# Performance work log

Hardware: AMD Instinct MI355X
Metric: run time of the kernel (lower is better)

## Reference

```python
import jax, jax.numpy as jnp
import numpy as np

N_NODES = 50000
N_EDGES = 640000
IN_DIM = 128
HID = 128
OUT_DIM = 16
BATCH = 2
EPS = 1e-5


def setup_inputs() -> dict:
    key = jax.random.key(0)
    ks = jax.random.split(key, 12)
    x = jax.random.normal(ks[0], (BATCH, N_NODES, IN_DIM), dtype=jnp.float32)
    edge_index = jax.random.randint(ks[1], (2, N_EDGES), 0, N_NODES, dtype=jnp.int32)
    # learned per-edge log-weights (initialized ~0 like nn.Parameter(zeros), small noise for a nontrivial test)
    edge_weight_param = 0.01 * jax.random.normal(ks[2], (N_EDGES,), dtype=jnp.float32)
    s1 = 1.0 / np.sqrt(IN_DIM)
    s2 = 1.0 / np.sqrt(HID)
    W1 = jax.random.uniform(ks[3], (IN_DIM, HID), minval=-s1, maxval=s1, dtype=jnp.float32)
    b1 = jnp.zeros((HID,), jnp.float32)
    W2 = jax.random.uniform(ks[4], (HID, HID), minval=-s2, maxval=s2, dtype=jnp.float32)
    b2 = jnp.zeros((HID,), jnp.float32)
    g1 = jnp.ones((HID,), jnp.float32); be1 = jnp.zeros((HID,), jnp.float32)
    g2 = jnp.ones((HID,), jnp.float32); be2 = jnp.zeros((HID,), jnp.float32)
    Wc = jax.random.uniform(ks[5], (HID, OUT_DIM), minval=-s2, maxval=s2, dtype=jnp.float32)
    bc = jax.random.uniform(ks[6], (OUT_DIM,), minval=-s2, maxval=s2, dtype=jnp.float32)
    return {"x": x, "edge_index": edge_index, "edge_weight_param": edge_weight_param,
            "W1": W1, "b1": b1, "W2": W2, "b2": b2,
            "g1": g1, "be1": be1, "g2": g2, "be2": be2,
            "Wc": Wc, "bc": bc}


def _gcn_norm(edge_index, edge_weight):
    # PyG GCNConv: add self-loops (weight 1), symmetric D^-1/2 A D^-1/2 normalization
    row = jnp.concatenate([edge_index[0], jnp.arange(N_NODES, dtype=edge_index.dtype)])
    col = jnp.concatenate([edge_index[1], jnp.arange(N_NODES, dtype=edge_index.dtype)])
    ew = jnp.concatenate([edge_weight, jnp.ones((N_NODES,), edge_weight.dtype)])
    deg = jax.ops.segment_sum(ew, col, num_segments=N_NODES)
    dinv = jnp.where(deg > 0, jax.lax.rsqrt(jnp.maximum(deg, 1e-30)), 0.0)
    norm = dinv[row] * ew * dinv[col]
    return row, col, norm


def _gcn_conv(x, W, b, row, col, norm):
    # x: [B, N, F_in] -> [B, N, F_out]; gather-scale-scatter over edges
    xw = x @ W                                   # [B, N, H]
    msg = xw[:, row, :] * norm[None, :, None]    # [B, E+N, H]
    out = jax.vmap(lambda m: jax.ops.segment_sum(m, col, num_segments=N_NODES))(msg)
    return out + b


def _batchnorm(h, gamma, beta):
    # training-mode BN over flattened (B*N) rows, biased variance, eps=1e-5
    B, N, F = h.shape
    hf = h.reshape(-1, F)
    mu = hf.mean(axis=0)
    var = hf.var(axis=0)
    return (((hf - mu) * jax.lax.rsqrt(var + EPS)) * gamma + beta).reshape(B, N, F)


def reference(x, edge_index, edge_weight_param, W1, b1, W2, b2, g1, be1, g2, be2, Wc, bc):
    edge_weight = jnp.exp(edge_weight_param)  # learned exp edge weights
    row, col, norm = _gcn_norm(edge_index, edge_weight)
    h = jax.nn.relu(_gcn_conv(x, W1, b1, row, col, norm))
    h = _batchnorm(h, g1, be1)
    # dropout is identity in eval / deterministic reference
    h = jax.nn.relu(_gcn_conv(h, W2, b2, row, col, norm))
    h = _batchnorm(h, g2, be2)
    return h @ Wc + bc  # [B, N, OUT_DIM]
```

## Files before the change

### kernel.cpp

```cpp
#include <hip/hip_runtime.h>
#include <hip/hip_bf16.h>
#include <cstdint>
#include <cstddef>

#define N_NODES 50000
#define N_EDGES 640000
#define ROWS    100000
#define HID     128
#define OUTD    16
#define AGG_BLOCKS 2048
#define MID_BLOCKS 32
#define SCAN_BLOCKS 196
#define GEMM_BLOCKS 512
#define GEMM_TILES  (ROWS / 16)

typedef __attribute__((ext_vector_type(8))) uint16_t ushort8;
typedef __attribute__((ext_vector_type(8))) __bf16   bf16x8;
typedef __attribute__((ext_vector_type(4))) float    floatx4;

union FragU { ushort8 u; bf16x8 b; };

__device__ __forceinline__ float bf_lo(uint32_t u){
  union { uint32_t u; float f; } c; c.u = u << 16; return c.f;
}
__device__ __forceinline__ float bf_hi(uint32_t u){
  union { uint32_t u; float f; } c; c.u = u & 0xffff0000u; return c.f;
}
__device__ __forceinline__ uint16_t f2bf(float f){
  union { float f; uint32_t u; } c; c.f = f;
  uint32_t u = c.u;
  uint32_t r = (u + 0x7fffu + ((u >> 16) & 1u)) >> 16;
  return (uint16_t)r;
}

__global__ void k_init(unsigned long long* __restrict__ dc){
  int i = blockIdx.x * 256 + threadIdx.x;
  if (i < N_NODES) dc[i] = 0ull;
}

__global__ void k_edge1(const int* __restrict__ ei, const float* __restrict__ ewp,
                        unsigned long long* __restrict__ dc){
  int e = blockIdx.x * 256 + threadIdx.x;
  if (e < N_EDGES){
    float w = expf(ewp[e]);
    int c = ei[N_EDGES + e];
    unsigned long long inc = (1ull << 44) | (unsigned long long)(w * 1048576.0f + 0.5f);
    atomicAdd(&dc[c], inc);
  }
}

__global__ void k_scan_bsum(const unsigned long long* __restrict__ dc, int* __restrict__ bsum,
                            float* __restrict__ dinv){
  __shared__ int sd[256];
  int tid = threadIdx.x;
  int i = blockIdx.x * 256 + tid;
  int cnt = 0;
  if (i < N_NODES){
    unsigned long long v = dc[i];
    cnt = (int)(v >> 44);
    float deg = 1.0f + (float)((double)(v & ((1ull << 44) - 1)) * (1.0 / 1048576.0));
    dinv[i] = 1.0f / sqrtf(deg);
  }
  sd[tid] = cnt;
  __syncthreads();
  for (int off = 128; off > 0; off >>= 1){
    if (tid < off) sd[tid] += sd[tid + off];
    __syncthreads();
  }
  if (tid == 0) bsum[blockIdx.x] = sd[0];
}

__global__ void k_scan_excl(int* __restrict__ bsum){
  __shared__ int sd[256];
  int tid = threadIdx.x;
  sd[tid] = (tid < SCAN_BLOCKS) ? bsum[tid] : 0;
  __syncthreads();
  if (tid == 0){
    int run = 0;
    for (int i = 0; i < SCAN_BLOCKS; i++){ int t = sd[i]; sd[i] = run; run += t; }
  }
  __syncthreads();
  if (tid < SCAN_BLOCKS) bsum[tid] = sd[tid];
}

__global__ void k_scan_write(const unsigned long long* __restrict__ dc, const int* __restrict__ bsum,
                             int* __restrict__ rp, int* __restrict__ cur){
  __shared__ int sd[256];
  int tid = threadIdx.x;
  int i = blockIdx.x * 256 + tid;
  int v = (i < N_NODES) ? (int)(dc[i] >> 44) : 0;
  sd[tid] = v;
  __syncthreads();
  for (int off = 1; off < 256; off <<= 1){
    int t = (tid >= off) ? sd[tid - off] : 0;
    __syncthreads();
    sd[tid] += t;
    __syncthreads();
  }
  if (i < N_NODES){
    int r = bsum[blockIdx.x] + sd[tid] - v;
    rp[i] = r;
    cur[i] = r;
  }
  if (blockIdx.x == 0 && tid == 0) rp[N_NODES] = N_EDGES;
}

__global__ void k_fill(const int* __restrict__ ei, const float* __restrict__ ewp,
                       const float* __restrict__ dinv, int* __restrict__ cur,
                       unsigned long long* __restrict__ edg){
  int e = blockIdx.x * 256 + threadIdx.x;
  if (e < N_EDGES){
    int r = ei[e];
    int c = ei[N_EDGES + e];
    float w = expf(ewp[e]);
    float nrm = dinv[r] * w * dinv[c];
    int p = atomicAdd(&cur[c], 1);
    edg[p] = ((unsigned long long)__float_as_uint(nrm) << 32) | (unsigned int)r;
  }
}

__global__ void k_wpack(const float* __restrict__ W, const float* __restrict__ sca,
                        uint16_t* __restrict__ WP){
  int t = blockIdx.x * 256 + threadIdx.x;
  int L = t & 63;
  int s = (t >> 6) & 3;
  int c = t >> 8;
  int n = c * 16 + (L & 15);
  int k0 = s * 32 + (L >> 4) * 8;
  ushort8 r;
#pragma unroll
  for (int j = 0; j < 8; j++){
    float w = W[(size_t)(k0 + j) * HID + n];
    if (sca) w *= sca[k0 + j];
    r[j] = f2bf(w);
  }
  *((ushort8*)(WP + (size_t)t * 8)) = r;
}

__global__ void k_wpackc(const float* __restrict__ Wc, const float* __restrict__ sca,
                         uint16_t* __restrict__ WPC){
  int t = threadIdx.x;
  int L = t & 63;
  int s = t >> 6;
  int n = L & 15;
  int k0 = s * 32 + (L >> 4) * 8;
  ushort8 r;
#pragma unroll
  for (int j = 0; j < 8; j++)
    r[j] = f2bf(sca[k0 + j] * Wc[(size_t)(k0 + j) * OUTD + n]);
  *((ushort8*)(WPC + (size_t)t * 8)) = r;
}

__global__ void k_cvec(const float* __restrict__ shf, const float* __restrict__ W,
                       const float* __restrict__ bias, float* __restrict__ cv, int ncol, int stride){
  int j = threadIdx.x;
  if (j < ncol){
    float a = bias ? bias[j] : 0.f;
    for (int k = 0; k < HID; k++) a = fmaf(shf[k], W[(size_t)k * stride + j], a);
    cv[j] = a;
  }
}

template <bool FP32_IN>
__global__ __launch_bounds__(256, 2) void k_gemm_mfma(const void* __restrict__ Xv,
                                                      const uint16_t* __restrict__ WP,
                                                      uint16_t* __restrict__ Y){
  const int lane = threadIdx.x & 63;
  const int wid  = threadIdx.x >> 6;
  const int gw   = blockIdx.x * 4 + wid;
  const int nw   = GEMM_BLOCKS * 4;
  const int m    = lane & 15;
  const int kq   = lane >> 4;

  FragU wf[8][4];
#pragma unroll
  for (int c = 0; c < 8; c++)
#pragma unroll
    for (int s = 0; s < 4; s++)
      wf[c][s].u = *((const ushort8*)(WP + (size_t)(((c * 4 + s) * 64 + lane) * 8)));

  for (int t = gw; t < GEMM_TILES; t += nw){
    const int row0 = t * 16;
    FragU af[4];
    if (FP32_IN){
      const float* X = (const float*)Xv;
#pragma unroll
      for (int s = 0; s < 4; s++){
        const float* p = X + (size_t)(row0 + m) * HID + s * 32 + kq * 8;
        floatx4 f0 = *((const floatx4*)p);
        floatx4 f1 = *((const floatx4*)(p + 4));
        ushort8 r;
#pragma unroll
        for (int j = 0; j < 4; j++){ r[j] = f2bf(f0[j]); r[j + 4] = f2bf(f1[j]); }
        af[s].u = r;
      }
    } else {
      const uint16_t* X = (const uint16_t*)Xv;
#pragma unroll
      for (int s = 0; s < 4; s++)
        af[s].u = *((const ushort8*)(X + (size_t)(row0 + m) * HID + s * 32 + kq * 8));
    }

    floatx4 acc[8];
#pragma unroll
    for (int c = 0; c < 8; c++) acc[c] = floatx4{0.f, 0.f, 0.f, 0.f};
#pragma unroll
    for (int s = 0; s < 4; s++)
#pragma unroll
      for (int c = 0; c < 8; c++)
        acc[c] = __builtin_amdgcn_mfma_f32_16x16x32_bf16(af[s].b, wf[c][s].b, acc[c], 0, 0, 0);

#pragma unroll
    for (int c = 0; c < 8; c++)
#pragma unroll
      for (int i = 0; i < 4; i++)
        Y[(size_t)(row0 + kq * 4 + i) * HID + c * 16 + m] = f2bf(acc[c][i]);
  }
}

__global__ __launch_bounds__(256) void k_cls_mfma(const uint16_t* __restrict__ H,
                                                  const uint16_t* __restrict__ WPC,
                                                  const float* __restrict__ cvec,
                                                  float* __restrict__ out){
  const int lane = threadIdx.x & 63;
  const int wid  = threadIdx.x >> 6;
  const int gw   = blockIdx.x * 4 + wid;
  const int nw   = GEMM_BLOCKS * 4;
  const int m    = lane & 15;
  const int kq   = lane >> 4;

  FragU wf[4];
#pragma unroll
  for (int s = 0; s < 4; s++)
    wf[s].u = *((const ushort8*)(WPC + (size_t)((s * 64 + lane) * 8)));
  const float cv = cvec[m];

  for (int t = gw; t < GEMM_TILES; t += nw){
    const int row0 = t * 16;
    FragU af[4];
#pragma unroll
    for (int s = 0; s < 4; s++)
      af[s].u = *((const ushort8*)(H + (size_t)(row0 + m) * HID + s * 32 + kq * 8));
    floatx4 acc = floatx4{0.f, 0.f, 0.f, 0.f};
#pragma unroll
    for (int s = 0; s < 4; s++)
      acc = __builtin_amdgcn_mfma_f32_16x16x32_bf16(af[s].b, wf[s].b, acc, 0, 0, 0);
#pragma unroll
    for (int i = 0; i < 4; i++)
      out[(size_t)(row0 + kq * 4 + i) * OUTD + m] = acc[i] + cv;
  }
}

__global__ __launch_bounds__(256) void k_agg(const uint16_t* __restrict__ XW,
                                             const int* __restrict__ rp,
                                             const unsigned long long* __restrict__ edg,
                                             const float* __restrict__ dinv,
                                             const float* __restrict__ bias,
                                             const float* __restrict__ cvec,
                                             uint16_t* __restrict__ H,
                                             float* __restrict__ psum,
                                             float* __restrict__ pssq){
  __shared__ float lsum[128];
  __shared__ float lssq[128];
  const int tid = threadIdx.x;
  if (tid < 128){ lsum[tid] = 0.f; lssq[tid] = 0.f; }
  __syncthreads();

  const int lane = tid & 63;
  const int wid  = tid >> 6;
  const int gw   = blockIdx.x * 4 + wid;
  const int nw   = AGG_BLOCKS * 4;
  const uint32_t* Xu = (const uint32_t*)XW;
  uint32_t* Hu = (uint32_t*)H;
  const int f0 = lane * 2;
  const float b0 = bias[f0], b1 = bias[f0 + 1];
  const float c0 = cvec ? cvec[f0] : 0.f;
  const float c1 = cvec ? cvec[f0 + 1] : 0.f;
  float ts0 = 0.f, ts1 = 0.f, tq0 = 0.f, tq1 = 0.f;

  for (int node = gw; node < N_NODES; node += nw){
    const float di = dinv[node];
    const float sn = di * di;
    const int e0 = rp[node], e1 = rp[node + 1];
    uint32_t s0 = Xu[(size_t)node * 64 + lane];
    uint32_t s1 = Xu[(size_t)(N_NODES + node) * 64 + lane];
    float a0x = sn * bf_lo(s0), a0y = sn * bf_hi(s0);
    float a1x = sn * bf_lo(s1), a1y = sn * bf_hi(s1);
    float wsum = sn;
    int e = e0;
    for (; e + 8 <= e1; e += 8){
      unsigned long long rec[8];
#pragma unroll
      for (int u = 0; u < 8; u++) rec[u] = edg[e + u];
      uint32_t q0[8], q1[8];
#pragma unroll
      for (int u = 0; u < 8; u++){
        size_t src = (uint32_t)rec[u];
        q0[u] = Xu[src * 64 + lane];
        q1[u] = Xu[(N_NODES + src) * 64 + lane];
      }
#pragma unroll
      for (int u = 0; u < 8; u++){
        float w = __uint_as_float((uint32_t)(rec[u] >> 32));
        a0x = fmaf(w, bf_lo(q0[u]), a0x); a0y = fmaf(w, bf_hi(q0[u]), a0y);
        a1x = fmaf(w, bf_lo(q1[u]), a1x); a1y = fmaf(w, bf_hi(q1[u]), a1y);
        wsum += w;
      }
    }
    for (; e + 4 <= e1; e += 4){
      unsigned long long rec[4];
#pragma unroll
      for (int u = 0; u < 4; u++) rec[u] = edg[e + u];
      uint32_t q0[4], q1[4];
#pragma unroll
      for (int u = 0; u < 4; u++){
        size_t src = (uint32_t)rec[u];
        q0[u] = Xu[src * 64 + lane];
        q1[u] = Xu[(N_NODES + src) * 64 + lane];
      }
#pragma unroll
      for (int u = 0; u < 4; u++){
        float w = __uint_as_float((uint32_t)(rec[u] >> 32));
        a0x = fmaf(w, bf_lo(q0[u]), a0x); a0y = fmaf(w, bf_hi(q0[u]), a0y);
        a1x = fmaf(w, bf_lo(q1[u]), a1x); a1y = fmaf(w, bf_hi(q1[u]), a1y);
        wsum += w;
      }
    }
    for (; e < e1; e++){
      unsigned long long rec = edg[e];
      size_t src = (uint32_t)rec;
      float w = __uint_as_float((uint32_t)(rec >> 32));
      uint32_t g0 = Xu[src * 64 + lane];
      uint32_t g1 = Xu[(N_NODES + src) * 64 + lane];
      a0x = fmaf(w, bf_lo(g0), a0x); a0y = fmaf(w, bf_hi(g0), a0y);
      a1x = fmaf(w, bf_lo(g1), a1x); a1y = fmaf(w, bf_hi(g1), a1y);
      wsum += w;
    }
    a0x = fmaxf(fmaf(wsum, c0, a0x) + b0, 0.f); a0y = fmaxf(fmaf(wsum, c1, a0y) + b1, 0.f);
    a1x = fmaxf(fmaf(wsum, c0, a1x) + b0, 0.f); a1y = fmaxf(fmaf(wsum, c1, a1y) + b1, 0.f);
    Hu[(size_t)node * 64 + lane]             = (uint32_t)f2bf(a0x) | ((uint32_t)f2bf(a0y) << 16);
    Hu[(size_t)(N_NODES + node) * 64 + lane] = (uint32_t)f2bf(a1x) | ((uint32_t)f2bf(a1y) << 16);
    ts0 += a0x + a1x; ts1 += a0y + a1y;
    tq0 += a0x * a0x + a1x * a1x; tq1 += a0y * a0y + a1y * a1y;
  }

  atomicAdd(&lsum[f0],     ts0); atomicAdd(&lsum[f0 + 1], ts1);
  atomicAdd(&lssq[f0],     tq0); atomicAdd(&lssq[f0 + 1], tq1);
  __syncthreads();
  if (tid < 128){
    psum[(size_t)blockIdx.x * 128 + tid] = lsum[tid];
    pssq[(size_t)blockIdx.x * 128 + tid] = lssq[tid];
  }
}

__global__ __launch_bounds__(256) void k_bnmid(const float* __restrict__ psum,
                                               const float* __restrict__ pssq,
                                               float* __restrict__ msum,
                                               float* __restrict__ mssq){
  __shared__ float ss[2][128];
  __shared__ float sq[2][128];
  const int tid = threadIdx.x;
  const int f  = tid & 127;
  const int sl = tid >> 7;
  const int rows_per = AGG_BLOCKS / MID_BLOCKS;
  const int base = blockIdx.x * rows_per;
  float s = 0.f, q = 0.f;
  for (int r = base + sl; r < base + rows_per; r += 2){
    s += psum[(size_t)r * 128 + f];
    q += pssq[(size_t)r * 128 + f];
  }
  ss[sl][f] = s; sq[sl][f] = q;
  __syncthreads();
  if (tid < 128){
    msum[(size_t)blockIdx.x * 128 + tid] = ss[0][tid] + ss[1][tid];
    mssq[(size_t)blockIdx.x * 128 + tid] = sq[0][tid] + sq[1][tid];
  }
}

__global__ __launch_bounds__(128) void k_bnfin(const float* __restrict__ msum,
                                               const float* __restrict__ mssq,
                                               const float* __restrict__ gamma,
                                               const float* __restrict__ beta,
                                               float* __restrict__ sca,
                                               float* __restrict__ shf){
  const int f = threadIdx.x;
  float S = 0.f, Q = 0.f;
#pragma unroll
  for (int b = 0; b < MID_BLOCKS; b++){
    S += msum[(size_t)b * 128 + f];
    Q += mssq[(size_t)b * 128 + f];
  }
  const float inv = 1.0f / (float)ROWS;
  float mu = S * inv;
  float var = fmaxf(Q * inv - mu * mu, 0.f);
  float rstd = 1.0f / sqrtf(var + 1e-5f);
  float sc = gamma[f] * rstd;
  sca[f] = sc;
  shf[f] = fmaf(-mu, sc, beta[f]);
}

extern "C" void kernel_launch(void* const* d_in, const int* in_sizes, int n_in,
                              void* d_out, int out_size, void* d_ws, size_t ws_size,
                              hipStream_t stream){
  const float* x   = (const float*)d_in[0];
  const int*   ei  = (const int*)d_in[1];
  const float* ewp = (const float*)d_in[2];
  const float* W1  = (const float*)d_in[3];
  const float* b1  = (const float*)d_in[4];
  const float* W2  = (const float*)d_in[5];
  const float* b2  = (const float*)d_in[6];
  const float* g1  = (const float*)d_in[7];
  const float* be1 = (const float*)d_in[8];
  const float* g2  = (const float*)d_in[9];
  const float* be2 = (const float*)d_in[10];
  const float* Wc  = (const float*)d_in[11];
  const float* bc  = (const float*)d_in[12];
  float* out = (float*)d_out;

  char* wsb = (char*)d_ws;
  size_t off = 0;
  auto give = [&](size_t bytes) -> void* {
    void* p = wsb + off;
    off = (off + bytes + 255) & ~(size_t)255;
    return p;
  };
  uint16_t* XW  = (uint16_t*)give((size_t)ROWS * 128 * 2);
  uint16_t* Hb  = (uint16_t*)give((size_t)ROWS * 128 * 2);
  unsigned long long* DC  = (unsigned long long*)give((size_t)N_NODES * 8);
  unsigned long long* EDG = (unsigned long long*)give((size_t)N_EDGES * 8);
  float* DINV   = (float*)give((size_t)N_NODES * 4);
  int*   RP     = (int*)give((size_t)(N_NODES + 1) * 4);
  int*   CUR    = (int*)give((size_t)N_NODES * 4);
  int*   BSUM   = (int*)give(1024);
  float* PSUM   = (float*)give((size_t)AGG_BLOCKS * 128 * 4);
  float* PSSQ   = (float*)give((size_t)AGG_BLOCKS * 128 * 4);
  float* MSUM   = (float*)give((size_t)MID_BLOCKS * 128 * 4);
  float* MSSQ   = (float*)give((size_t)MID_BLOCKS * 128 * 4);
  float* SCA1   = (float*)give(512);
  float* SHF1   = (float*)give(512);
  float* SCA2   = (float*)give(512);
  float* SHF2   = (float*)give(512);
  uint16_t* WP1 = (uint16_t*)give((size_t)HID * HID * 2);
  uint16_t* WP2 = (uint16_t*)give((size_t)HID * HID * 2);
  uint16_t* WPC = (uint16_t*)give((size_t)HID * OUTD * 2);
  float* C2     = (float*)give(512);
  float* CVC    = (float*)give(64);
  (void)ws_size; (void)n_in; (void)in_sizes; (void)out_size;

  const int nb_nodes = (N_NODES + 255) / 256;
  const int nb_edges = (N_EDGES + 255) / 256;

  k_init<<<nb_nodes, 256, 0, stream>>>(DC);
  k_edge1<<<nb_edges, 256, 0, stream>>>(ei, ewp, DC);
  k_scan_bsum<<<SCAN_BLOCKS, 256, 0, stream>>>(DC, BSUM, DINV);
  k_scan_excl<<<1, 256, 0, stream>>>(BSUM);
  k_scan_write<<<SCAN_BLOCKS, 256, 0, stream>>>(DC, BSUM, RP, CUR);
  k_fill<<<nb_edges, 256, 0, stream>>>(ei, ewp, DINV, CUR, EDG);
  k_wpack<<<8, 256, 0, stream>>>(W1, nullptr, WP1);

  k_gemm_mfma<true><<<GEMM_BLOCKS, 256, 0, stream>>>(x, WP1, XW);
  k_agg<<<AGG_BLOCKS, 256, 0, stream>>>(XW, RP, EDG, DINV, b1, nullptr, Hb, PSUM, PSSQ);
  k_bnmid<<<MID_BLOCKS, 256, 0, stream>>>(PSUM, PSSQ, MSUM, MSSQ);
  k_bnfin<<<1, 128, 0, stream>>>(MSUM, MSSQ, g1, be1, SCA1, SHF1);

  k_wpack<<<8, 256, 0, stream>>>(W2, SCA1, WP2);
  k_cvec<<<1, 128, 0, stream>>>(SHF1, W2, nullptr, C2, HID, HID);
  k_gemm_mfma<false><<<GEMM_BLOCKS, 256, 0, stream>>>(Hb, WP2, XW);
  k_agg<<<AGG_BLOCKS, 256, 0, stream>>>(XW, RP, EDG, DINV, b2, C2, Hb, PSUM, PSSQ);
  k_bnmid<<<MID_BLOCKS, 256, 0, stream>>>(PSUM, PSSQ, MSUM, MSSQ);
  k_bnfin<<<1, 128, 0, stream>>>(MSUM, MSSQ, g2, be2, SCA2, SHF2);

  k_wpackc<<<1, 256, 0, stream>>>(Wc, SCA2, WPC);
  k_cvec<<<1, 128, 0, stream>>>(SHF2, Wc, bc, CVC, OUTD, OUTD);
  k_cls_mfma<<<GEMM_BLOCKS, 256, 0, stream>>>(Hb, WPC, CVC, out);
}
```

Measured before the change: 380.4 us.

## Interleave batch features per node in XW and precompute CSR slots from degree atomics

The GEMM now writes its output with both batch rows of a node interleaved, so each node's 256 bf16 values sit together. The aggregation kernel can then fetch both batches of a source node with one 8-byte load per lane instead of two separate 4-byte gathers from distant rows. Separately, the degree-count atomic returns each edge's old count as its slot within the node's segment. This removes the second atomic pass over a cursor array in the CSR fill, at the cost of a per-edge slot buffer. The classifier GEMM keeps the old row-major tiling of the hidden output.

```diff
diff --git a/kernel.cpp b/kernel.cpp
--- a/kernel.cpp
+++ b/kernel.cpp
@@ -12,7 +12,8 @@
 #define MID_BLOCKS 32
 #define SCAN_BLOCKS 196
 #define GEMM_BLOCKS 512
-#define GEMM_TILES  (ROWS / 16)
+#define GEMM_TILES  (N_NODES / 8)
+#define CLS_TILES   (ROWS / 16)
 
 typedef __attribute__((ext_vector_type(8))) uint16_t ushort8;
 typedef __attribute__((ext_vector_type(8))) __bf16   bf16x8;
@@ -33,19 +34,21 @@
   return (uint16_t)r;
 }
 
+
 __global__ void k_init(unsigned long long* __restrict__ dc){
   int i = blockIdx.x * 256 + threadIdx.x;
   if (i < N_NODES) dc[i] = 0ull;
 }
 
 __global__ void k_edge1(const int* __restrict__ ei, const float* __restrict__ ewp,
-                        unsigned long long* __restrict__ dc){
+                        unsigned long long* __restrict__ dc, unsigned int* __restrict__ slot){
   int e = blockIdx.x * 256 + threadIdx.x;
   if (e < N_EDGES){
     float w = expf(ewp[e]);
     int c = ei[N_EDGES + e];
     unsigned long long inc = (1ull << 44) | (unsigned long long)(w * 1048576.0f + 0.5f);
-    atomicAdd(&dc[c], inc);
+    unsigned long long old = atomicAdd(&dc[c], inc);
+    slot[e] = (unsigned int)(old >> 44);
   }
 }
 
@@ -84,7 +87,7 @@
 }
 
 __global__ void k_scan_write(const unsigned long long* __restrict__ dc, const int* __restrict__ bsum,
-                             int* __restrict__ rp, int* __restrict__ cur){
+                             int* __restrict__ rp){
   __shared__ int sd[256];
   int tid = threadIdx.x;
   int i = blockIdx.x * 256 + tid;
@@ -97,24 +100,20 @@
     sd[tid] += t;
     __syncthreads();
   }
-  if (i < N_NODES){
-    int r = bsum[blockIdx.x] + sd[tid] - v;
-    rp[i] = r;
-    cur[i] = r;
-  }
+  if (i < N_NODES) rp[i] = bsum[blockIdx.x] + sd[tid] - v;
   if (blockIdx.x == 0 && tid == 0) rp[N_NODES] = N_EDGES;
 }
 
 __global__ void k_fill(const int* __restrict__ ei, const float* __restrict__ ewp,
-                       const float* __restrict__ dinv, int* __restrict__ cur,
-                       unsigned long long* __restrict__ edg){
+                       const float* __restrict__ dinv, const unsigned int* __restrict__ slot,
+                       const int* __restrict__ rp, unsigned long long* __restrict__ edg){
   int e = blockIdx.x * 256 + threadIdx.x;
   if (e < N_EDGES){
     int r = ei[e];
     int c = ei[N_EDGES + e];
     float w = expf(ewp[e]);
     float nrm = dinv[r] * w * dinv[c];
-    int p = atomicAdd(&cur[c], 1);
+    int p = rp[c] + (int)slot[e];
     edg[p] = ((unsigned long long)__float_as_uint(nrm) << 32) | (unsigned int)r;
   }
 }
@@ -180,13 +179,14 @@
       wf[c][s].u = *((const ushort8*)(WP + (size_t)(((c * 4 + s) * 64 + lane) * 8)));
 
   for (int t = gw; t < GEMM_TILES; t += nw){
-    const int row0 = t * 16;
+    const int n0 = t * 8;
+    const size_t ga = (size_t)((m & 1) * N_NODES + n0 + (m >> 1)) * HID;
     FragU af[4];
     if (FP32_IN){
       const float* X = (const float*)Xv;
 #pragma unroll
       for (int s = 0; s < 4; s++){
-        const float* p = X + (size_t)(row0 + m) * HID + s * 32 + kq * 8;
+        const float* p = X + ga + s * 32 + kq * 8;
         floatx4 f0 = *((const floatx4*)p);
         floatx4 f1 = *((const floatx4*)(p + 4));
         ushort8 r;
@@ -198,7 +198,7 @@
       const uint16_t* X = (const uint16_t*)Xv;
 #pragma unroll
       for (int s = 0; s < 4; s++)
-        af[s].u = *((const ushort8*)(X + (size_t)(row0 + m) * HID + s * 32 + kq * 8));
+        af[s].u = *((const ushort8*)(X + ga + s * 32 + kq * 8));
     }
 
     floatx4 acc[8];
@@ -213,8 +213,12 @@
 #pragma unroll
     for (int c = 0; c < 8; c++)
 #pragma unroll
-      for (int i = 0; i < 4; i++)
-        Y[(size_t)(row0 + kq * 4 + i) * HID + c * 16 + m] = f2bf(acc[c][i]);
+      for (int i = 0; i < 4; i++){
+        int rr = kq * 4 + i;
+        int node = n0 + (rr >> 1);
+        int b = rr & 1;
+        Y[(size_t)node * 256 + (size_t)(c * 8 + (m >> 1)) * 4 + b * 2 + (m & 1)] = f2bf(acc[c][i]);
+      }
   }
 }
 
@@ -235,7 +239,7 @@
     wf[s].u = *((const ushort8*)(WPC + (size_t)((s * 64 + lane) * 8)));
   const float cv = cvec[m];
 
-  for (int t = gw; t < GEMM_TILES; t += nw){
+  for (int t = gw; t < CLS_TILES; t += nw){
     const int row0 = t * 16;
     FragU af[4];
 #pragma unroll
@@ -282,28 +286,26 @@
     const float di = dinv[node];
     const float sn = di * di;
     const int e0 = rp[node], e1 = rp[node + 1];
-    uint32_t s0 = Xu[(size_t)node * 64 + lane];
-    uint32_t s1 = Xu[(size_t)(N_NODES + node) * 64 + lane];
-    float a0x = sn * bf_lo(s0), a0y = sn * bf_hi(s0);
-    float a1x = sn * bf_lo(s1), a1y = sn * bf_hi(s1);
+    uint2 sp = *((const uint2*)(Xu + (size_t)node * 128 + lane * 2));
+    float a0x = sn * bf_lo(sp.x), a0y = sn * bf_hi(sp.x);
+    float a1x = sn * bf_lo(sp.y), a1y = sn * bf_hi(sp.y);
     float wsum = sn;
     int e = e0;
     for (; e + 8 <= e1; e += 8){
       unsigned long long rec[8];
 #pragma unroll
       for (int u = 0; u < 8; u++) rec[u] = edg[e + u];
-      uint32_t q0[8], q1[8];
+      uint2 q[8];
 #pragma unroll
       for (int u = 0; u < 8; u++){
         size_t src = (uint32_t)rec[u];
-        q0[u] = Xu[src * 64 + lane];
-        q1[u] = Xu[(N_NODES + src) * 64 + lane];
+        q[u] = *((const uint2*)(Xu + src * 128 + lane * 2));
       }
 #pragma unroll
       for (int u = 0; u < 8; u++){
         float w = __uint_as_float((uint32_t)(rec[u] >> 32));
-        a0x = fmaf(w, bf_lo(q0[u]), a0x); a0y = fmaf(w, bf_hi(q0[u]), a0y);
-        a1x = fmaf(w, bf_lo(q1[u]), a1x); a1y = fmaf(w, bf_hi(q1[u]), a1y);
+        a0x = fmaf(w, bf_lo(q[u].x), a0x); a0y = fmaf(w, bf_hi(q[u].x), a0y);
+        a1x = fmaf(w, bf_lo(q[u].y), a1x); a1y = fmaf(w, bf_hi(q[u].y), a1y);
         wsum += w;
       }
     }
@@ -311,18 +313,17 @@
       unsigned long long rec[4];
 #pragma unroll
       for (int u = 0; u < 4; u++) rec[u] = edg[e + u];
-      uint32_t q0[4], q1[4];
+      uint2 q[4];
 #pragma unroll
       for (int u = 0; u < 4; u++){
         size_t src = (uint32_t)rec[u];
-        q0[u] = Xu[src * 64 + lane];
-        q1[u] = Xu[(N_NODES + src) * 64 + lane];
+        q[u] = *((const uint2*)(Xu + src * 128 + lane * 2));
       }
 #pragma unroll
       for (int u = 0; u < 4; u++){
         float w = __uint_as_float((uint32_t)(rec[u] >> 32));
-        a0x = fmaf(w, bf_lo(q0[u]), a0x); a0y = fmaf(w, bf_hi(q0[u]), a0y);
-        a1x = fmaf(w, bf_lo(q1[u]), a1x); a1y = fmaf(w, bf_hi(q1[u]), a1y);
+        a0x = fmaf(w, bf_lo(q[u].x), a0x); a0y = fmaf(w, bf_hi(q[u].x), a0y);
+        a1x = fmaf(w, bf_lo(q[u].y), a1x); a1y = fmaf(w, bf_hi(q[u].y), a1y);
         wsum += w;
       }
     }
@@ -330,10 +331,9 @@
       unsigned long long rec = edg[e];
       size_t src = (uint32_t)rec;
       float w = __uint_as_float((uint32_t)(rec >> 32));
-      uint32_t g0 = Xu[src * 64 + lane];
-      uint32_t g1 = Xu[(N_NODES + src) * 64 + lane];
-      a0x = fmaf(w, bf_lo(g0), a0x); a0y = fmaf(w, bf_hi(g0), a0y);
-      a1x = fmaf(w, bf_lo(g1), a1x); a1y = fmaf(w, bf_hi(g1), a1y);
+      uint2 q = *((const uint2*)(Xu + src * 128 + lane * 2));
+      a0x = fmaf(w, bf_lo(q.x), a0x); a0y = fmaf(w, bf_hi(q.x), a0y);
+      a1x = fmaf(w, bf_lo(q.y), a1x); a1y = fmaf(w, bf_hi(q.y), a1y);
       wsum += w;
     }
     a0x = fmaxf(fmaf(wsum, c0, a0x) + b0, 0.f); a0y = fmaxf(fmaf(wsum, c1, a0y) + b1, 0.f);
@@ -428,9 +428,9 @@
   uint16_t* Hb  = (uint16_t*)give((size_t)ROWS * 128 * 2);
   unsigned long long* DC  = (unsigned long long*)give((size_t)N_NODES * 8);
   unsigned long long* EDG = (unsigned long long*)give((size_t)N_EDGES * 8);
+  unsigned int* SLOT = (unsigned int*)give((size_t)N_EDGES * 4);
   float* DINV   = (float*)give((size_t)N_NODES * 4);
   int*   RP     = (int*)give((size_t)(N_NODES + 1) * 4);
-  int*   CUR    = (int*)give((size_t)N_NODES * 4);
   int*   BSUM   = (int*)give(1024);
   float* PSUM   = (float*)give((size_t)AGG_BLOCKS * 128 * 4);
   float* PSSQ   = (float*)give((size_t)AGG_BLOCKS * 128 * 4);
@@ -451,11 +451,11 @@
   const int nb_edges = (N_EDGES + 255) / 256;
 
   k_init<<<nb_nodes, 256, 0, stream>>>(DC);
-  k_edge1<<<nb_edges, 256, 0, stream>>>(ei, ewp, DC);
+  k_edge1<<<nb_edges, 256, 0, stream>>>(ei, ewp, DC, SLOT);
   k_scan_bsum<<<SCAN_BLOCKS, 256, 0, stream>>>(DC, BSUM, DINV);
   k_scan_excl<<<1, 256, 0, stream>>>(BSUM);
-  k_scan_write<<<SCAN_BLOCKS, 256, 0, stream>>>(DC, BSUM, RP, CUR);
-  k_fill<<<nb_edges, 256, 0, stream>>>(ei, ewp, DINV, CUR, EDG);
+  k_scan_write<<<SCAN_BLOCKS, 256, 0, stream>>>(DC, BSUM, RP);
+  k_fill<<<nb_edges, 256, 0, stream>>>(ei, ewp, DINV, SLOT, RP, EDG);
   k_wpack<<<8, 256, 0, stream>>>(W1, nullptr, WP1);
 
   k_gemm_mfma<true><<<GEMM_BLOCKS, 256, 0, stream>>>(x, WP1, XW);
```

New measurement: 378.9 us. Within noise of the previous version (-0.4%).

## Reuse degree-atomic return as CSR slot, pack GEMM output stores, prefetch next node in aggregation

Applied to the files above, without the earlier changes.

The edge-count atomic now returns its old count as each edge's slot within its destination bucket. The fill kernel computes positions from the row pointer plus that slot, which removes the second atomic pass over a cursor array. The weight packing is permuted so that each lane owns two adjacent output columns, letting the GEMM store 32-bit pairs instead of 16-bit scalars. The aggregation loop prefetches the next node's row pointers, dinv and self features while it processes the current node, and a 2-edge tail loop is added. These steps cost an extra edge-sized slot buffer and more live registers in the aggregation kernel.

```diff
diff --git a/kernel.cpp b/kernel.cpp
--- a/kernel.cpp
+++ b/kernel.cpp
@@ -39,13 +39,14 @@
 }
 
 __global__ void k_edge1(const int* __restrict__ ei, const float* __restrict__ ewp,
-                        unsigned long long* __restrict__ dc){
+                        unsigned long long* __restrict__ dc, unsigned int* __restrict__ slot){
   int e = blockIdx.x * 256 + threadIdx.x;
   if (e < N_EDGES){
     float w = expf(ewp[e]);
     int c = ei[N_EDGES + e];
     unsigned long long inc = (1ull << 44) | (unsigned long long)(w * 1048576.0f + 0.5f);
-    atomicAdd(&dc[c], inc);
+    unsigned long long old = atomicAdd(&dc[c], inc);
+    slot[e] = (unsigned int)(old >> 44);
   }
 }
 
@@ -84,7 +85,7 @@
 }
 
 __global__ void k_scan_write(const unsigned long long* __restrict__ dc, const int* __restrict__ bsum,
-                             int* __restrict__ rp, int* __restrict__ cur){
+                             int* __restrict__ rp){
   __shared__ int sd[256];
   int tid = threadIdx.x;
   int i = blockIdx.x * 256 + tid;
@@ -97,24 +98,20 @@
     sd[tid] += t;
     __syncthreads();
   }
-  if (i < N_NODES){
-    int r = bsum[blockIdx.x] + sd[tid] - v;
-    rp[i] = r;
-    cur[i] = r;
-  }
+  if (i < N_NODES) rp[i] = bsum[blockIdx.x] + sd[tid] - v;
   if (blockIdx.x == 0 && tid == 0) rp[N_NODES] = N_EDGES;
 }
 
 __global__ void k_fill(const int* __restrict__ ei, const float* __restrict__ ewp,
-                       const float* __restrict__ dinv, int* __restrict__ cur,
-                       unsigned long long* __restrict__ edg){
+                       const float* __restrict__ dinv, const unsigned int* __restrict__ slot,
+                       const int* __restrict__ rp, unsigned long long* __restrict__ edg){
   int e = blockIdx.x * 256 + threadIdx.x;
   if (e < N_EDGES){
     int r = ei[e];
     int c = ei[N_EDGES + e];
     float w = expf(ewp[e]);
     float nrm = dinv[r] * w * dinv[c];
-    int p = atomicAdd(&cur[c], 1);
+    int p = rp[c] + (int)slot[e];
     edg[p] = ((unsigned long long)__float_as_uint(nrm) << 32) | (unsigned int)r;
   }
 }
@@ -125,7 +122,7 @@
   int L = t & 63;
   int s = (t >> 6) & 3;
   int c = t >> 8;
-  int n = c * 16 + (L & 15);
+  int n = (c >> 1) * 32 + 2 * (L & 15) + (c & 1);
   int k0 = s * 32 + (L >> 4) * 8;
   ushort8 r;
 #pragma unroll
@@ -179,6 +176,7 @@
     for (int s = 0; s < 4; s++)
       wf[c][s].u = *((const ushort8*)(WP + (size_t)(((c * 4 + s) * 64 + lane) * 8)));
 
+  uint32_t* Yu = (uint32_t*)Y;
   for (int t = gw; t < GEMM_TILES; t += nw){
     const int row0 = t * 16;
     FragU af[4];
@@ -211,10 +209,12 @@
         acc[c] = __builtin_amdgcn_mfma_f32_16x16x32_bf16(af[s].b, wf[c][s].b, acc[c], 0, 0, 0);
 
 #pragma unroll
-    for (int c = 0; c < 8; c++)
-#pragma unroll
-      for (int i = 0; i < 4; i++)
-        Y[(size_t)(row0 + kq * 4 + i) * HID + c * 16 + m] = f2bf(acc[c][i]);
+    for (int t4 = 0; t4 < 4; t4++)
+#pragma unroll
+      for (int i = 0; i < 4; i++){
+        uint32_t pr = (uint32_t)f2bf(acc[2 * t4][i]) | ((uint32_t)f2bf(acc[2 * t4 + 1][i]) << 16);
+        Yu[(size_t)(row0 + kq * 4 + i) * 64 + t4 * 16 + m] = pr;
+      }
   }
 }
 
@@ -278,70 +278,99 @@
   const float c1 = cvec ? cvec[f0 + 1] : 0.f;
   float ts0 = 0.f, ts1 = 0.f, tq0 = 0.f, tq1 = 0.f;
 
-  for (int node = gw; node < N_NODES; node += nw){
-    const float di = dinv[node];
-    const float sn = di * di;
-    const int e0 = rp[node], e1 = rp[node + 1];
+  int node = gw;
+  if (node < N_NODES){
+    int e0 = rp[node], e1 = rp[node + 1];
+    float di = dinv[node];
     uint32_t s0 = Xu[(size_t)node * 64 + lane];
     uint32_t s1 = Xu[(size_t)(N_NODES + node) * 64 + lane];
-    float a0x = sn * bf_lo(s0), a0y = sn * bf_hi(s0);
-    float a1x = sn * bf_lo(s1), a1y = sn * bf_hi(s1);
-    float wsum = sn;
-    int e = e0;
-    for (; e + 8 <= e1; e += 8){
-      unsigned long long rec[8];
-#pragma unroll
-      for (int u = 0; u < 8; u++) rec[u] = edg[e + u];
-      uint32_t q0[8], q1[8];
-#pragma unroll
-      for (int u = 0; u < 8; u++){
-        size_t src = (uint32_t)rec[u];
-        q0[u] = Xu[src * 64 + lane];
-        q1[u] = Xu[(N_NODES + src) * 64 + lane];
-      }
-#pragma unroll
-      for (int u = 0; u < 8; u++){
-        float w = __uint_as_float((uint32_t)(rec[u] >> 32));
-        a0x = fmaf(w, bf_lo(q0[u]), a0x); a0y = fmaf(w, bf_hi(q0[u]), a0y);
-        a1x = fmaf(w, bf_lo(q1[u]), a1x); a1y = fmaf(w, bf_hi(q1[u]), a1y);
+    while (true){
+      const int nn = node + nw;
+      const bool more = (nn < N_NODES);
+      int ne0 = 0, ne1 = 0; float ndi = 0.f; uint32_t ns0 = 0, ns1 = 0;
+      if (more){
+        ne0 = rp[nn]; ne1 = rp[nn + 1];
+        ndi = dinv[nn];
+        ns0 = Xu[(size_t)nn * 64 + lane];
+        ns1 = Xu[(size_t)(N_NODES + nn) * 64 + lane];
+      }
+
+      const float sn = di * di;
+      float a0x = sn * bf_lo(s0), a0y = sn * bf_hi(s0);
+      float a1x = sn * bf_lo(s1), a1y = sn * bf_hi(s1);
+      float wsum = sn;
+      int e = e0;
+      for (; e + 8 <= e1; e += 8){
+        unsigned long long rec[8];
+#pragma unroll
+        for (int u = 0; u < 8; u++) rec[u] = edg[e + u];
+        uint32_t q0[8], q1[8];
+#pragma unroll
+        for (int u = 0; u < 8; u++){
+          size_t src = (uint32_t)rec[u];
+          q0[u] = Xu[src * 64 + lane];
+          q1[u] = Xu[(N_NODES + src) * 64 + lane];
+        }
+#pragma unroll
+        for (int u = 0; u < 8; u++){
+          float w = __uint_as_float((uint32_t)(rec[u] >> 32));
+          a0x = fmaf(w, bf_lo(q0[u]), a0x); a0y = fmaf(w, bf_hi(q0[u]), a0y);
+          a1x = fmaf(w, bf_lo(q1[u]), a1x); a1y = fmaf(w, bf_hi(q1[u]), a1y);
+          wsum += w;
+        }
+      }
+      for (; e + 4 <= e1; e += 4){
+        unsigned long long rec[4];
+#pragma unroll
+        for (int u = 0; u < 4; u++) rec[u] = edg[e + u];
+        uint32_t q0[4], q1[4];
+#pragma unroll
+        for (int u = 0; u < 4; u++){
+          size_t src = (uint32_t)rec[u];
+          q0[u] = Xu[src * 64 + lane];
+          q1[u] = Xu[(N_NODES + src) * 64 + lane];
+        }
+#pragma unroll
+        for (int u = 0; u < 4; u++){
+          float w = __uint_as_float((uint32_t)(rec[u] >> 32));
+          a0x = fmaf(w, bf_lo(q0[u]), a0x); a0y = fmaf(w, bf_hi(q0[u]), a0y);
+          a1x = fmaf(w, bf_lo(q1[u]), a1x); a1y = fmaf(w, bf_hi(q1[u]), a1y);
+          wsum += w;
+        }
+      }
+      for (; e + 2 <= e1; e += 2){
+        unsigned long long ra = edg[e], rb = edg[e + 1];
+        size_t sa = (uint32_t)ra, sb = (uint32_t)rb;
+        uint32_t qa0 = Xu[sa * 64 + lane], qa1 = Xu[(N_NODES + sa) * 64 + lane];
+        uint32_t qb0 = Xu[sb * 64 + lane], qb1 = Xu[(N_NODES + sb) * 64 + lane];
+        float wa = __uint_as_float((uint32_t)(ra >> 32));
+        float wb = __uint_as_float((uint32_t)(rb >> 32));
+        a0x = fmaf(wa, bf_lo(qa0), a0x); a0y = fmaf(wa, bf_hi(qa0), a0y);
+        a1x = fmaf(wa, bf_lo(qa1), a1x); a1y = fmaf(wa, bf_hi(qa1), a1y);
+        a0x = fmaf(wb, bf_lo(qb0), a0x); a0y = fmaf(wb, bf_hi(qb0), a0y);
+        a1x = fmaf(wb, bf_lo(qb1), a1x); a1y = fmaf(wb, bf_hi(qb1), a1y);
+        wsum += wa + wb;
+      }
+      for (; e < e1; e++){
+        unsigned long long rec = edg[e];
+        size_t src = (uint32_t)rec;
+        float w = __uint_as_float((uint32_t)(rec >> 32));
+        uint32_t g0 = Xu[src * 64 + lane];
+        uint32_t g1 = Xu[(N_NODES + src) * 64 + lane];
+        a0x = fmaf(w, bf_lo(g0), a0x); a0y = fmaf(w, bf_hi(g0), a0y);
+        a1x = fmaf(w, bf_lo(g1), a1x); a1y = fmaf(w, bf_hi(g1), a1y);
         wsum += w;
       }
+      a0x = fmaxf(fmaf(wsum, c0, a0x) + b0, 0.f); a0y = fmaxf(fmaf(wsum, c1, a0y) + b1, 0.f);
+      a1x = fmaxf(fmaf(wsum, c0, a1x) + b0, 0.f); a1y = fmaxf(fmaf(wsum, c1, a1y) + b1, 0.f);
+      Hu[(size_t)node * 64 + lane]             = (uint32_t)f2bf(a0x) | ((uint32_t)f2bf(a0y) << 16);
+      Hu[(size_t)(N_NODES + node) * 64 + lane] = (uint32_t)f2bf(a1x) | ((uint32_t)f2bf(a1y) << 16);
+      ts0 += a0x + a1x; ts1 += a0y + a1y;
+      tq0 += a0x * a0x + a1x * a1x; tq1 += a0y * a0y + a1y * a1y;
+
+      if (!more) break;
+      node = nn; e0 = ne0; e1 = ne1; di = ndi; s0 = ns0; s1 = ns1;
     }
-    for (; e + 4 <= e1; e += 4){
-      unsigned long long rec[4];
-#pragma unroll
-      for (int u = 0; u < 4; u++) rec[u] = edg[e + u];
-      uint32_t q0[4], q1[4];
-#pragma unroll
-      for (int u = 0; u < 4; u++){
-        size_t src = (uint32_t)rec[u];
-        q0[u] = Xu[src * 64 + lane];
-        q1[u] = Xu[(N_NODES + src) * 64 + lane];
-      }
-#pragma unroll
-      for (int u = 0; u < 4; u++){
-        float w = __uint_as_float((uint32_t)(rec[u] >> 32));
-        a0x = fmaf(w, bf_lo(q0[u]), a0x); a0y = fmaf(w, bf_hi(q0[u]), a0y);
-        a1x = fmaf(w, bf_lo(q1[u]), a1x); a1y = fmaf(w, bf_hi(q1[u]), a1y);
-        wsum += w;
-      }
-    }
-    for (; e < e1; e++){
-      unsigned long long rec = edg[e];
-      size_t src = (uint32_t)rec;
-      float w = __uint_as_float((uint32_t)(rec >> 32));
-      uint32_t g0 = Xu[src * 64 + lane];
-      uint32_t g1 = Xu[(N_NODES + src) * 64 + lane];
-      a0x = fmaf(w, bf_lo(g0), a0x); a0y = fmaf(w, bf_hi(g0), a0y);
-      a1x = fmaf(w, bf_lo(g1), a1x); a1y = fmaf(w, bf_hi(g1), a1y);
-      wsum += w;
-    }
-    a0x = fmaxf(fmaf(wsum, c0, a0x) + b0, 0.f); a0y = fmaxf(fmaf(wsum, c1, a0y) + b1, 0.f);
-    a1x = fmaxf(fmaf(wsum, c0, a1x) + b0, 0.f); a1y = fmaxf(fmaf(wsum, c1, a1y) + b1, 0.f);
-    Hu[(size_t)node * 64 + lane]             = (uint32_t)f2bf(a0x) | ((uint32_t)f2bf(a0y) << 16);
-    Hu[(size_t)(N_NODES + node) * 64 + lane] = (uint32_t)f2bf(a1x) | ((uint32_t)f2bf(a1y) << 16);
-    ts0 += a0x + a1x; ts1 += a0y + a1y;
-    tq0 += a0x * a0x + a1x * a1x; tq1 += a0y * a0y + a1y * a1y;
   }
 
   atomicAdd(&lsum[f0],     ts0); atomicAdd(&lsum[f0 + 1], ts1);
@@ -428,9 +457,9 @@
   uint16_t* Hb  = (uint16_t*)give((size_t)ROWS * 128 * 2);
   unsigned long long* DC  = (unsigned long long*)give((size_t)N_NODES * 8);
   unsigned long long* EDG = (unsigned long long*)give((size_t)N_EDGES * 8);
+  unsigned int* SLOT = (unsigned int*)give((size_t)N_EDGES * 4);
   float* DINV   = (float*)give((size_t)N_NODES * 4);
   int*   RP     = (int*)give((size_t)(N_NODES + 1) * 4);
-  int*   CUR    = (int*)give((size_t)N_NODES * 4);
   int*   BSUM   = (int*)give(1024);
   float* PSUM   = (float*)give((size_t)AGG_BLOCKS * 128 * 4);
   float* PSSQ   = (float*)give((size_t)AGG_BLOCKS * 128 * 4);
@@ -451,11 +480,11 @@
   const int nb_edges = (N_EDGES + 255) / 256;
 
   k_init<<<nb_nodes, 256, 0, stream>>>(DC);
-  k_edge1<<<nb_edges, 256, 0, stream>>>(ei, ewp, DC);
+  k_edge1<<<nb_edges, 256, 0, stream>>>(ei, ewp, DC, SLOT);
   k_scan_bsum<<<SCAN_BLOCKS, 256, 0, stream>>>(DC, BSUM, DINV);
   k_scan_excl<<<1, 256, 0, stream>>>(BSUM);
-  k_scan_write<<<SCAN_BLOCKS, 256, 0, stream>>>(DC, BSUM, RP, CUR);
-  k_fill<<<nb_edges, 256, 0, stream>>>(ei, ewp, DINV, CUR, EDG);
+  k_scan_write<<<SCAN_BLOCKS, 256, 0, stream>>>(DC, BSUM, RP);
+  k_fill<<<nb_edges, 256, 0, stream>>>(ei, ewp, DINV, SLOT, RP, EDG);
   k_wpack<<<8, 256, 0, stream>>>(W1, nullptr, WP1);
 
   k_gemm_mfma<true><<<GEMM_BLOCKS, 256, 0, stream>>>(x, WP1, XW);
```

New measurement: 359.0 us. 1.06x faster.
